# Kernel tuning notes

Hardware: AMD Instinct MI355X
Metric: run time of the kernel (lower is better)

## Reference

```python
import jax, jax.numpy as jnp
import numpy as np

IN_CH = 256
OUT_CH = 64
HEADS = 8


def setup_inputs() -> dict:
    key = jax.random.key(0)
    ks = jax.random.split(key, 7)
    N = 4096
    proj = OUT_CH * HEADS
    s_in = 1.0 / np.sqrt(IN_CH)
    return {
        "query_input": jax.random.normal(ks[0], (N, IN_CH), dtype=jnp.float32),
        "Wq": jax.random.uniform(ks[1], (proj, IN_CH), jnp.float32, -s_in, s_in),
        "bq": jax.random.uniform(ks[2], (proj,), jnp.float32, -s_in, s_in),
        "Wk": jax.random.uniform(ks[3], (proj, IN_CH), jnp.float32, -s_in, s_in),
        "bk": jax.random.uniform(ks[4], (proj,), jnp.float32, -s_in, s_in),
        "Wv": jax.random.uniform(ks[5], (proj, IN_CH), jnp.float32, -s_in, s_in),
        "bv": jax.random.uniform(ks[6], (proj,), jnp.float32, -s_in, s_in),
    }


def reference(query_input, Wq, bq, Wk, bk, Wv, bv):
    N = query_input.shape[0]
    # projections -> [N, H, M]
    q = (query_input @ Wq.T + bq).reshape(N, HEADS, OUT_CH)
    k = (query_input @ Wk.T + bk).reshape(N, HEADS, OUT_CH)
    v = (query_input @ Wv.T + bv).reshape(N, HEADS, OUT_CH)
    # sigmoid attention scores [N, L, H]
    attention_num = jax.nn.sigmoid(jnp.einsum('nhm,lhm->nlh', q, k))
    # sum-normalization over L (keys)
    normalizer = attention_num.sum(axis=1, keepdims=True)  # [N, 1, H]
    attention = attention_num / normalizer
    # weighted V reduction [N, H, D], then mean over heads -> [N, D]
    out = jnp.einsum('nlh,lhd->nhd', attention, v).mean(axis=1)
    return out
```

## Files before the change

### kernel.cpp

```cpp
#include <hip/hip_runtime.h>
#include <hip/hip_bf16.h>
#include <math.h>

#define N_TOK 4096
#define IN_CH 256
#define OUT_CH 64
#define HEADS 8
#define PROJ (OUT_CH * HEADS)
#define NLOG2E -1.44269504088896340736f

typedef float f32x4 __attribute__((ext_vector_type(4)));
typedef __bf16 bf16x8 __attribute__((ext_vector_type(8)));
typedef unsigned short ushort_t;

__device__ inline ushort_t bf16rne(float x) {
    unsigned u = __float_as_uint(x);
    unsigned r = (u + 0x7FFFu + ((u >> 16) & 1u)) >> 16;
    return (ushort_t)r;
}

__global__ __launch_bounds__(256) void cast_pack_kernel(
    const float* __restrict__ X,
    const float* __restrict__ Wq, const float* __restrict__ Wk,
    const float* __restrict__ Wv,
    ushort_t* __restrict__ Xa, ushort_t* __restrict__ Wp)
{
    const int i = blockIdx.x * 256 + threadIdx.x;
    const float* src;
    ushort_t* dst;
    float scale = 1.0f;
    if (i < 131072) {
        const int t = i & 15, quad = (i >> 4) & 3, k8 = (i >> 6) & 7, g = i >> 9;
        src = X + (size_t)(g * 16 + t) * IN_CH + k8 * 32 + quad * 8;
        dst = Xa + (size_t)i * 8;
    } else {
        const int j = i - 131072;
        const int z = j >> 14;
        const int r = j & 16383;
        const int cl = r & 15, quad = (r >> 4) & 3, k8 = (r >> 6) & 7, gc = r >> 9;
        const float* W = (z == 0) ? Wq : (z == 1) ? Wk : Wv;
        src = W + (size_t)(gc * 16 + cl) * IN_CH + k8 * 32 + quad * 8;
        dst = Wp + (size_t)z * 131072 * 8 + (size_t)r * 8;
        if (z == 0) scale = NLOG2E;
    }
    float4 a = *(const float4*)src;
    float4 b = *(const float4*)(src + 4);
    ushort_t pk[8];
    pk[0] = bf16rne(a.x * scale); pk[1] = bf16rne(a.y * scale);
    pk[2] = bf16rne(a.z * scale); pk[3] = bf16rne(a.w * scale);
    pk[4] = bf16rne(b.x * scale); pk[5] = bf16rne(b.y * scale);
    pk[6] = bf16rne(b.z * scale); pk[7] = bf16rne(b.w * scale);
    *(uint4*)dst = *(uint4*)pk;
}

__global__ __launch_bounds__(256) void proj_mfma_kernel(
    const ushort_t* __restrict__ Xa, const ushort_t* __restrict__ Wp,
    const float* __restrict__ bq, const float* __restrict__ bk,
    const float* __restrict__ bv,
    ushort_t* __restrict__ Qb, ushort_t* __restrict__ Kb,
    ushort_t* __restrict__ Vt)
{
    const int z = blockIdx.z;
    const float* bias = (z == 0) ? bq : (z == 1) ? bk : bv;
    const float bscale = (z == 0) ? NLOG2E : 1.0f;
    const int c0 = blockIdx.x * 64;
    const int n0 = blockIdx.y * 64;

    const int tid = threadIdx.x;
    const int w = tid >> 6;
    const int lane = tid & 63;
    const int l15 = lane & 15;
    const int quad = lane >> 4;

    __shared__ ushort_t Es[64 * 68];

    const ushort_t* xa = Xa + (size_t)(blockIdx.y * 4 + w) * 4096 + quad * 128 + l15 * 8;
    const ushort_t* wp0 = Wp + (size_t)z * 131072 * 8 +
                          (size_t)(blockIdx.x * 4) * 4096 + quad * 128 + l15 * 8;

    f32x4 acc[4] = {{0.f, 0.f, 0.f, 0.f}, {0.f, 0.f, 0.f, 0.f},
                    {0.f, 0.f, 0.f, 0.f}, {0.f, 0.f, 0.f, 0.f}};

#pragma unroll 2
    for (int k8 = 0; k8 < 8; ++k8) {
        bf16x8 a = *(const bf16x8*)(xa + k8 * 512);
#pragma unroll
        for (int f = 0; f < 4; ++f) {
            bf16x8 b = *(const bf16x8*)(wp0 + f * 4096 + k8 * 512);
            acc[f] = __builtin_amdgcn_mfma_f32_16x16x32_bf16(a, b, acc[f], 0, 0, 0);
        }
    }

    if (z < 2) {
#pragma unroll
        for (int f = 0; f < 4; ++f) {
            const float bb = bias[c0 + f * 16 + l15] * bscale;
#pragma unroll
            for (int r = 0; r < 4; ++r)
                Es[(w * 16 + quad * 4 + r) * 68 + f * 16 + l15] = bf16rne(acc[f][r] + bb);
        }
    } else {
#pragma unroll
        for (int f = 0; f < 4; ++f) {
            const float bb = bias[c0 + f * 16 + l15];
#pragma unroll
            for (int r = 0; r < 4; ++r)
                Es[(f * 16 + l15) * 68 + w * 16 + quad * 4 + r] = bf16rne(acc[f][r] + bb);
        }
    }
    __syncthreads();

    const int erow = tid >> 2;
    const int ecol = (tid & 3) * 16;
    uint4 pk0 = *(uint4*)&Es[erow * 68 + ecol];
    uint4 pk1 = *(uint4*)&Es[erow * 68 + ecol + 8];
    if (z < 2) {
        ushort_t* out = z ? Kb : Qb;
        ushort_t* p = &out[(size_t)(n0 + erow) * PROJ + c0 + ecol];
        *(uint4*)p = pk0;
        *(uint4*)(p + 8) = pk1;
    } else {
        ushort_t* p = &Vt[(size_t)(c0 + erow) * N_TOK + n0 + ecol];
        *(uint4*)p = pk0;
        *(uint4*)(p + 8) = pk1;
    }
}

__global__ __launch_bounds__(256, 4) void attn_kernel(
    const ushort_t* __restrict__ Qb, const ushort_t* __restrict__ Kb,
    const ushort_t* __restrict__ Vt,
    float* __restrict__ NUM, float* __restrict__ DEN)
{
    const int h = blockIdx.y;
    const int z = blockIdx.z;
    const int n0 = blockIdx.x * 64;
    const int tid = threadIdx.x;
    const int w = tid >> 6;
    const int lane = tid & 63;
    const int l15 = lane & 15;
    const int quad = lane >> 4;

    __shared__ ushort_t Ks[64 * 64];
    __shared__ ushort_t Vs[64 * 64];
    __shared__ ushort_t Ps[4][16 * 72];

    bf16x8 qb[2];
    {
        const ushort_t* base = Qb + (size_t)(n0 + w * 16 + l15) * PROJ + h * 64 + quad * 8;
        qb[0] = *(const bf16x8*)(base);
        qb[1] = *(const bf16x8*)(base + 32);
    }

    bf16x8 onesv;
#pragma unroll
    for (int j = 0; j < 8; ++j) onesv[j] = (__bf16)1.0f;

    f32x4 o[4] = {{0.f, 0.f, 0.f, 0.f}, {0.f, 0.f, 0.f, 0.f},
                  {0.f, 0.f, 0.f, 0.f}, {0.f, 0.f, 0.f, 0.f}};
    f32x4 dacc = {0.f, 0.f, 0.f, 0.f};

    const int srow = tid >> 2;
    const int sc2 = (tid & 3) * 2;
    const int sp0 = (sc2 ^ (srow & 7)) * 8;
    const int sp1 = ((sc2 + 1) ^ (srow & 7)) * 8;
    const int xm = l15 & 7;
    const int rofA = (quad ^ xm) * 8;
    const int rofB = ((4 + quad) ^ xm) * 8;

    const ushort_t* kgp = Kb + (size_t)h * 64 + sc2 * 8 +
                          (size_t)(z * 2048 + srow) * PROJ;
    const ushort_t* vgp = Vt + (size_t)h * 64 * N_TOK + (size_t)srow * N_TOK +
                          sc2 * 8 + z * 2048;

    uint4 kr0 = ((const uint4*)kgp)[0], kr1 = ((const uint4*)kgp)[1];
    uint4 vr0 = ((const uint4*)vgp)[0], vr1 = ((const uint4*)vgp)[1];

    for (int lt = 0; lt < 32; ++lt) {
        __syncthreads();
        *(uint4*)&Ks[srow * 64 + sp0] = kr0;
        *(uint4*)&Ks[srow * 64 + sp1] = kr1;
        *(uint4*)&Vs[srow * 64 + sp0] = vr0;
        *(uint4*)&Vs[srow * 64 + sp1] = vr1;
        __syncthreads();

        if (lt < 31) {
            kgp += 64 * PROJ;
            vgp += 64;
            kr0 = ((const uint4*)kgp)[0]; kr1 = ((const uint4*)kgp)[1];
            vr0 = ((const uint4*)vgp)[0]; vr1 = ((const uint4*)vgp)[1];
        }

        f32x4 s[4] = {{0.f, 0.f, 0.f, 0.f}, {0.f, 0.f, 0.f, 0.f},
                      {0.f, 0.f, 0.f, 0.f}, {0.f, 0.f, 0.f, 0.f}};
#pragma unroll
        for (int f = 0; f < 4; ++f) {
            bf16x8 ka = *(const bf16x8*)&Ks[(f * 16 + l15) * 64 + rofA];
            s[f] = __builtin_amdgcn_mfma_f32_16x16x32_bf16(ka, qb[0], s[f], 0, 0, 0);
        }
#pragma unroll
        for (int f = 0; f < 4; ++f) {
            bf16x8 ka = *(const bf16x8*)&Ks[(f * 16 + l15) * 64 + rofB];
            s[f] = __builtin_amdgcn_mfma_f32_16x16x32_bf16(ka, qb[1], s[f], 0, 0, 0);
        }

        ushort_t* pw = &Ps[w][l15 * 72];
#pragma unroll
        for (int f = 0; f < 4; ++f) {
            float p0 = __builtin_amdgcn_rcpf(1.0f + __builtin_amdgcn_exp2f(s[f][0]));
            float p1 = __builtin_amdgcn_rcpf(1.0f + __builtin_amdgcn_exp2f(s[f][1]));
            float p2 = __builtin_amdgcn_rcpf(1.0f + __builtin_amdgcn_exp2f(s[f][2]));
            float p3 = __builtin_amdgcn_rcpf(1.0f + __builtin_amdgcn_exp2f(s[f][3]));
            unsigned u0 = __float_as_uint(p0) + 0x8000u;
            unsigned u1 = __float_as_uint(p1) + 0x8000u;
            unsigned u2 = __float_as_uint(p2) + 0x8000u;
            unsigned u3 = __float_as_uint(p3) + 0x8000u;
            uint2 pk;
            pk.x = __builtin_amdgcn_perm(u1, u0, 0x07060302u);
            pk.y = __builtin_amdgcn_perm(u3, u2, 0x07060302u);
            *(uint2*)&pw[f * 16 + quad * 4] = pk;
        }

#pragma unroll
        for (int c = 0; c < 2; ++c) {
            bf16x8 pa = *(const bf16x8*)&Ps[w][l15 * 72 + c * 32 + quad * 8];
            const int rof = c ? rofB : rofA;
#pragma unroll
            for (int f = 0; f < 4; ++f) {
                bf16x8 vb = *(const bf16x8*)&Vs[(f * 16 + l15) * 64 + rof];
                o[f] = __builtin_amdgcn_mfma_f32_16x16x32_bf16(pa, vb, o[f], 0, 0, 0);
            }
            dacc = __builtin_amdgcn_mfma_f32_16x16x32_bf16(pa, onesv, dacc, 0, 0, 0);
        }
    }

#pragma unroll
    for (int f = 0; f < 4; ++f) {
#pragma unroll
        for (int r = 0; r < 4; ++r) {
            const int q = n0 + w * 16 + quad * 4 + r;
            NUM[((size_t)z * N_TOK + q) * PROJ + h * 64 + f * 16 + l15] = o[f][r];
        }
    }
    if (l15 == 0) {
#pragma unroll
        for (int r = 0; r < 4; ++r)
            DEN[((size_t)z * N_TOK + n0 + w * 16 + quad * 4 + r) * HEADS + h] = dacc[r];
    }
}

__global__ __launch_bounds__(256) void reduce_kernel(
    const float* __restrict__ NUM, const float* __restrict__ DEN,
    float* __restrict__ out)
{
    const int g = blockIdx.x * 256 + threadIdx.x;
    const int n = g >> 6;
    const int d = g & 63;
    float acc = 0.0f;
#pragma unroll
    for (int hh = 0; hh < HEADS; ++hh) {
        float num = NUM[(size_t)n * PROJ + hh * 64 + d] +
                    NUM[((size_t)N_TOK + n) * PROJ + hh * 64 + d];
        float dd = DEN[(size_t)n * HEADS + hh] +
                   DEN[((size_t)N_TOK + n) * HEADS + hh];
        acc += num / dd;
    }
    out[g] = acc * 0.125f;
}

extern "C" void kernel_launch(void* const* d_in, const int* in_sizes, int n_in,
                              void* d_out, int out_size, void* d_ws, size_t ws_size,
                              hipStream_t stream) {
    (void)in_sizes; (void)n_in; (void)out_size; (void)ws_size;
    const float* X  = (const float*)d_in[0];
    const float* Wq = (const float*)d_in[1];
    const float* bq = (const float*)d_in[2];
    const float* Wk = (const float*)d_in[3];
    const float* bk = (const float*)d_in[4];
    const float* Wv = (const float*)d_in[5];
    const float* bv = (const float*)d_in[6];
    float* out = (float*)d_out;

    float* NUM = (float*)d_ws;
    float* DEN = NUM + (size_t)2 * N_TOK * PROJ;
    ushort_t* Qb = (ushort_t*)(DEN + (size_t)2 * N_TOK * HEADS);
    ushort_t* Kb = Qb + (size_t)N_TOK * PROJ;
    ushort_t* Vt = Kb + (size_t)N_TOK * PROJ;
    ushort_t* Xa = Vt + (size_t)N_TOK * PROJ;
    ushort_t* Wp = Xa + (size_t)N_TOK * IN_CH;

    cast_pack_kernel<<<dim3(704), 256, 0, stream>>>(X, Wq, Wk, Wv, Xa, Wp);
    proj_mfma_kernel<<<dim3(PROJ / 64, N_TOK / 64, 3), 256, 0, stream>>>(
        Xa, Wp, bq, bk, bv, Qb, Kb, Vt);
    attn_kernel<<<dim3(N_TOK / 64, HEADS, 2), 256, 0, stream>>>(
        Qb, Kb, Vt, NUM, DEN);
    reduce_kernel<<<dim3(N_TOK * OUT_CH / 256), 256, 0, stream>>>(NUM, DEN, out);
}
```

Measured before the change: 143.2 us.

## Split attention key range four ways and accumulate partials with atomics

```diff
diff --git a/kernel.cpp b/kernel.cpp
--- a/kernel.cpp
+++ b/kernel.cpp
@@ -8,6 +8,7 @@
 #define HEADS 8
 #define PROJ (OUT_CH * HEADS)
 #define NLOG2E -1.44269504088896340736f
+#define ZSPLIT 4
 
 typedef float f32x4 __attribute__((ext_vector_type(4)));
 typedef __bf16 bf16x8 __attribute__((ext_vector_type(8)));
@@ -126,7 +127,7 @@
     }
 }
 
-__global__ __launch_bounds__(256, 4) void attn_kernel(
+__global__ __launch_bounds__(256, 6) void attn_kernel(
     const ushort_t* __restrict__ Qb, const ushort_t* __restrict__ Kb,
     const ushort_t* __restrict__ Vt,
     float* __restrict__ NUM, float* __restrict__ DEN)
@@ -168,14 +169,14 @@
     const int rofB = ((4 + quad) ^ xm) * 8;
 
     const ushort_t* kgp = Kb + (size_t)h * 64 + sc2 * 8 +
-                          (size_t)(z * 2048 + srow) * PROJ;
+                          (size_t)(z * 1024 + srow) * PROJ;
     const ushort_t* vgp = Vt + (size_t)h * 64 * N_TOK + (size_t)srow * N_TOK +
-                          sc2 * 8 + z * 2048;
+                          sc2 * 8 + z * 1024;
 
     uint4 kr0 = ((const uint4*)kgp)[0], kr1 = ((const uint4*)kgp)[1];
     uint4 vr0 = ((const uint4*)vgp)[0], vr1 = ((const uint4*)vgp)[1];
 
-    for (int lt = 0; lt < 32; ++lt) {
+    for (int lt = 0; lt < 16; ++lt) {
         __syncthreads();
         *(uint4*)&Ks[srow * 64 + sp0] = kr0;
         *(uint4*)&Ks[srow * 64 + sp1] = kr1;
@@ -183,7 +184,7 @@
         *(uint4*)&Vs[srow * 64 + sp1] = vr1;
         __syncthreads();
 
-        if (lt < 31) {
+        if (lt < 15) {
             kgp += 64 * PROJ;
             vgp += 64;
             kr0 = ((const uint4*)kgp)[0]; kr1 = ((const uint4*)kgp)[1];
@@ -210,13 +211,11 @@
             float p1 = __builtin_amdgcn_rcpf(1.0f + __builtin_amdgcn_exp2f(s[f][1]));
             float p2 = __builtin_amdgcn_rcpf(1.0f + __builtin_amdgcn_exp2f(s[f][2]));
             float p3 = __builtin_amdgcn_rcpf(1.0f + __builtin_amdgcn_exp2f(s[f][3]));
-            unsigned u0 = __float_as_uint(p0) + 0x8000u;
-            unsigned u1 = __float_as_uint(p1) + 0x8000u;
-            unsigned u2 = __float_as_uint(p2) + 0x8000u;
-            unsigned u3 = __float_as_uint(p3) + 0x8000u;
             uint2 pk;
-            pk.x = __builtin_amdgcn_perm(u1, u0, 0x07060302u);
-            pk.y = __builtin_amdgcn_perm(u3, u2, 0x07060302u);
+            pk.x = __builtin_amdgcn_perm(__float_as_uint(p1), __float_as_uint(p0),
+                                         0x07060302u);
+            pk.y = __builtin_amdgcn_perm(__float_as_uint(p3), __float_as_uint(p2),
+                                         0x07060302u);
             *(uint2*)&pw[f * 16 + quad * 4] = pk;
         }
 
@@ -238,13 +237,13 @@
 #pragma unroll
         for (int r = 0; r < 4; ++r) {
             const int q = n0 + w * 16 + quad * 4 + r;
-            NUM[((size_t)z * N_TOK + q) * PROJ + h * 64 + f * 16 + l15] = o[f][r];
+            atomicAdd(&NUM[(size_t)q * PROJ + h * 64 + f * 16 + l15], o[f][r]);
         }
     }
     if (l15 == 0) {
 #pragma unroll
         for (int r = 0; r < 4; ++r)
-            DEN[((size_t)z * N_TOK + n0 + w * 16 + quad * 4 + r) * HEADS + h] = dacc[r];
+            atomicAdd(&DEN[(size_t)(n0 + w * 16 + quad * 4 + r) * HEADS + h], dacc[r]);
     }
 }
 
@@ -257,13 +256,8 @@
     const int d = g & 63;
     float acc = 0.0f;
 #pragma unroll
-    for (int hh = 0; hh < HEADS; ++hh) {
-        float num = NUM[(size_t)n * PROJ + hh * 64 + d] +
-                    NUM[((size_t)N_TOK + n) * PROJ + hh * 64 + d];
-        float dd = DEN[(size_t)n * HEADS + hh] +
-                   DEN[((size_t)N_TOK + n) * HEADS + hh];
-        acc += num / dd;
-    }
+    for (int hh = 0; hh < HEADS; ++hh)
+        acc += NUM[(size_t)n * PROJ + hh * 64 + d] / DEN[(size_t)n * HEADS + hh];
     out[g] = acc * 0.125f;
 }
 
@@ -281,17 +275,18 @@
     float* out = (float*)d_out;
 
     float* NUM = (float*)d_ws;
-    float* DEN = NUM + (size_t)2 * N_TOK * PROJ;
-    ushort_t* Qb = (ushort_t*)(DEN + (size_t)2 * N_TOK * HEADS);
+    float* DEN = NUM + (size_t)N_TOK * PROJ;
+    ushort_t* Qb = (ushort_t*)(DEN + (size_t)N_TOK * HEADS);
     ushort_t* Kb = Qb + (size_t)N_TOK * PROJ;
     ushort_t* Vt = Kb + (size_t)N_TOK * PROJ;
     ushort_t* Xa = Vt + (size_t)N_TOK * PROJ;
     ushort_t* Wp = Xa + (size_t)N_TOK * IN_CH;
 
+    hipMemsetAsync(NUM, 0, (size_t)(N_TOK * PROJ + N_TOK * HEADS) * 4, stream);
     cast_pack_kernel<<<dim3(704), 256, 0, stream>>>(X, Wq, Wk, Wv, Xa, Wp);
     proj_mfma_kernel<<<dim3(PROJ / 64, N_TOK / 64, 3), 256, 0, stream>>>(
         Xa, Wp, bq, bk, bv, Qb, Kb, Vt);
-    attn_kernel<<<dim3(N_TOK / 64, HEADS, 2), 256, 0, stream>>>(
+    attn_kernel<<<dim3(N_TOK / 64, HEADS, ZSPLIT), 256, 0, stream>>>(
         Qb, Kb, Vt, NUM, DEN);
     reduce_kernel<<<dim3(N_TOK * OUT_CH / 256), 256, 0, stream>>>(NUM, DEN, out);
 }
```

After: 147.6 us. 3.1% more time.

## Fuse head/split reduction into attention kernel via last-block atomic ticket

Applied to the files above, without the earlier changes.

```diff
diff --git a/kernel.cpp b/kernel.cpp
--- a/kernel.cpp
+++ b/kernel.cpp
@@ -23,8 +23,11 @@
     const float* __restrict__ X,
     const float* __restrict__ Wq, const float* __restrict__ Wk,
     const float* __restrict__ Wv,
-    ushort_t* __restrict__ Xa, ushort_t* __restrict__ Wp)
+    ushort_t* __restrict__ Xa, ushort_t* __restrict__ Wp,
+    int* __restrict__ Tk)
 {
+    if (blockIdx.x == 0 && threadIdx.x < 64) Tk[threadIdx.x] = 0;
+
     const int i = blockIdx.x * 256 + threadIdx.x;
     const float* src;
     ushort_t* dst;
@@ -129,7 +132,8 @@
 __global__ __launch_bounds__(256, 4) void attn_kernel(
     const ushort_t* __restrict__ Qb, const ushort_t* __restrict__ Kb,
     const ushort_t* __restrict__ Vt,
-    float* __restrict__ NUM, float* __restrict__ DEN)
+    float* __restrict__ NUM, float* __restrict__ DEN,
+    float* __restrict__ out, int* __restrict__ Tk)
 {
     const int h = blockIdx.y;
     const int z = blockIdx.z;
@@ -143,6 +147,7 @@
     __shared__ ushort_t Ks[64 * 64];
     __shared__ ushort_t Vs[64 * 64];
     __shared__ ushort_t Ps[4][16 * 72];
+    __shared__ int is_last;
 
     bf16x8 qb[2];
     {
@@ -210,13 +215,11 @@
             float p1 = __builtin_amdgcn_rcpf(1.0f + __builtin_amdgcn_exp2f(s[f][1]));
             float p2 = __builtin_amdgcn_rcpf(1.0f + __builtin_amdgcn_exp2f(s[f][2]));
             float p3 = __builtin_amdgcn_rcpf(1.0f + __builtin_amdgcn_exp2f(s[f][3]));
-            unsigned u0 = __float_as_uint(p0) + 0x8000u;
-            unsigned u1 = __float_as_uint(p1) + 0x8000u;
-            unsigned u2 = __float_as_uint(p2) + 0x8000u;
-            unsigned u3 = __float_as_uint(p3) + 0x8000u;
             uint2 pk;
-            pk.x = __builtin_amdgcn_perm(u1, u0, 0x07060302u);
-            pk.y = __builtin_amdgcn_perm(u3, u2, 0x07060302u);
+            pk.x = __builtin_amdgcn_perm(__float_as_uint(p1), __float_as_uint(p0),
+                                         0x07060302u);
+            pk.y = __builtin_amdgcn_perm(__float_as_uint(p3), __float_as_uint(p2),
+                                         0x07060302u);
             *(uint2*)&pw[f * 16 + quad * 4] = pk;
         }
 
@@ -246,25 +249,29 @@
         for (int r = 0; r < 4; ++r)
             DEN[((size_t)z * N_TOK + n0 + w * 16 + quad * 4 + r) * HEADS + h] = dacc[r];
     }
-}
-
-__global__ __launch_bounds__(256) void reduce_kernel(
-    const float* __restrict__ NUM, const float* __restrict__ DEN,
-    float* __restrict__ out)
-{
-    const int g = blockIdx.x * 256 + threadIdx.x;
-    const int n = g >> 6;
-    const int d = g & 63;
-    float acc = 0.0f;
-#pragma unroll
-    for (int hh = 0; hh < HEADS; ++hh) {
-        float num = NUM[(size_t)n * PROJ + hh * 64 + d] +
-                    NUM[((size_t)N_TOK + n) * PROJ + hh * 64 + d];
-        float dd = DEN[(size_t)n * HEADS + hh] +
-                   DEN[((size_t)N_TOK + n) * HEADS + hh];
-        acc += num / dd;
-    }
-    out[g] = acc * 0.125f;
+
+    __threadfence();
+    __syncthreads();
+    if (tid == 0)
+        is_last = (atomicAdd(&Tk[blockIdx.x], 1) == 15);
+    __syncthreads();
+    if (is_last) {
+        __threadfence();
+        for (int i = tid; i < 64 * 64; i += 256) {
+            const int n = n0 + (i >> 6);
+            const int d = i & 63;
+            float acc = 0.0f;
+#pragma unroll
+            for (int hh = 0; hh < HEADS; ++hh) {
+                float num = NUM[(size_t)n * PROJ + hh * 64 + d] +
+                            NUM[((size_t)N_TOK + n) * PROJ + hh * 64 + d];
+                float dd = DEN[(size_t)n * HEADS + hh] +
+                           DEN[((size_t)N_TOK + n) * HEADS + hh];
+                acc += num * __builtin_amdgcn_rcpf(dd);
+            }
+            out[n * 64 + d] = acc * 0.125f;
+        }
+    }
 }
 
 extern "C" void kernel_launch(void* const* d_in, const int* in_sizes, int n_in,
@@ -282,16 +289,16 @@
 
     float* NUM = (float*)d_ws;
     float* DEN = NUM + (size_t)2 * N_TOK * PROJ;
-    ushort_t* Qb = (ushort_t*)(DEN + (size_t)2 * N_TOK * HEADS);
+    int*   Tk  = (int*)(DEN + (size_t)2 * N_TOK * HEADS);
+    ushort_t* Qb = (ushort_t*)(Tk + 64);
     ushort_t* Kb = Qb + (size_t)N_TOK * PROJ;
     ushort_t* Vt = Kb + (size_t)N_TOK * PROJ;
     ushort_t* Xa = Vt + (size_t)N_TOK * PROJ;
     ushort_t* Wp = Xa + (size_t)N_TOK * IN_CH;
 
-    cast_pack_kernel<<<dim3(704), 256, 0, stream>>>(X, Wq, Wk, Wv, Xa, Wp);
+    cast_pack_kernel<<<dim3(704), 256, 0, stream>>>(X, Wq, Wk, Wv, Xa, Wp, Tk);
     proj_mfma_kernel<<<dim3(PROJ / 64, N_TOK / 64, 3), 256, 0, stream>>>(
         Xa, Wp, bq, bk, bv, Qb, Kb, Vt);
     attn_kernel<<<dim3(N_TOK / 64, HEADS, 2), 256, 0, stream>>>(
-        Qb, Kb, Vt, NUM, DEN);
-    reduce_kernel<<<dim3(N_TOK * OUT_CH / 256), 256, 0, stream>>>(NUM, DEN, out);
-}
+        Qb, Kb, Vt, NUM, DEN, out, Tk);
+}
```

Result: slower. 270.0 us (+88.5%).
